# Performance work log

Hardware: AMD Instinct MI355X
Metric: run time of the kernel (lower is better)

The kernel has to match this reference:

```python
import jax, jax.numpy as jnp
import numpy as np

B, N, C = 16, 196608, 2

def setup_inputs() -> dict:
    key = jax.random.key(0)
    k1, k2, k3, k4, k5 = jax.random.split(key, 5)
    return {
        "r": jax.random.normal(k1, (B, N, C), dtype=jnp.float32),
        "w": jax.random.uniform(k2, (B, N, 2), dtype=jnp.float32),
        "J_p": jax.random.normal(k3, (B, N, C, 6), dtype=jnp.float32),
        "J_d": jax.random.uniform(k4, (B, N, C, 1), dtype=jnp.float32),
        "lmbda": jax.random.uniform(k5, (B, 1, 1), dtype=jnp.float32),
    }

def reference(r, w, J_p, J_d, lmbda):
    # r: (B,N,C)  w: (B,N,2)  J_p: (B,N,C,6)  J_d: (B,N,C,1)  lmbda: (B,1,1)
    conf = w[..., 0:1]                                  # (B,N,1)
    node_lambda = w[..., 1:2]                           # (B,N,1)
    conf4 = conf[..., None]                             # (B,N,1,1)
    Jd = J_d[..., 0]                                    # (B,N,C)

    # Gauss-Newton blocks (sum-over-N reductions of tiny outer products)
    H_pp = jnp.einsum('bnki,bnkj->bij', J_p, conf4 * J_p)        # (B,6,6)
    H_pd = jnp.einsum('bnki,bnkj->bnij', J_p, conf4 * J_d)       # (B,N,6,1)
    H_dd = jnp.einsum('bnk,bnk->bn', Jd, conf * Jd)[..., None]   # (B,N,1)
    wr = conf * r                                                # (B,N,C)
    g_p = jnp.einsum('bnki,bnk->bi', J_p, wr)[..., None]         # (B,6,1)
    g_d = jnp.einsum('bnk,bnk->bn', Jd, wr)[..., None]           # (B,N,1)

    eye6 = jnp.eye(6, dtype=H_pp.dtype)[None]                    # (1,6,6)
    H_pp = H_pp + lmbda * eye6                                   # LM damping on pose block

    # Depth block damping + safe inverse
    H_dd_safe = jnp.maximum(H_dd + lmbda + node_lambda, 1e-4)    # (B,N,1)
    inv_H_dd = 1.0 / H_dd_safe                                   # (B,N,1)

    # Schur complement: H_eff = H_pp - sum_n H_pd invHdd H_pd^T
    H_pd_invHdd = H_pd * inv_H_dd[..., None]                     # (B,N,6,1)
    term = jnp.einsum('bnik,bnjk->bij', H_pd_invHdd, H_pd)       # (B,6,6)
    H_eff = H_pp - term + (0.01 + 0.001) * eye6                  # eye*0.01 then ridge 0.001
    g_eff = g_p - jnp.sum(H_pd_invHdd * g_d[..., None], axis=1)  # (B,6,1)

    delta_pose = jnp.linalg.solve(H_eff, g_eff)                  # (B,6,1)
    dp = delta_pose[..., 0]                                      # (B,6)

    # Back-substitute depths
    v = jnp.einsum('bnij,bi->bnj', H_pd, dp)                     # (B,N,1)
    delta_depth = inv_H_dd * (g_d - v)                           # (B,N,1)

    delta_pose_out = jnp.clip(dp, -2.0, 2.0)                     # (B,6)
    return (delta_pose_out, delta_depth)
```

## Files before the change

### kernel.cpp

```cpp
#include <hip/hip_runtime.h>


constexpr int NACC = 27;

__device__ __forceinline__ void accum_point(
    float ja0, float ja1, float ja2, float ja3, float ja4, float ja5,
    float jb0, float jb1, float jb2, float jb3, float jb4, float jb5,
    float r0, float r1, float conf, float nlam, float jd0, float jd1,
    float lam, float* __restrict__ A, float* __restrict__ g)
{
    const float ja[6] = {ja0, ja1, ja2, ja3, ja4, ja5};
    const float jb[6] = {jb0, jb1, jb2, jb3, jb4, jb5};
    float h[6], gp[6];
#pragma unroll
    for (int i = 0; i < 6; ++i) {
        h[i]  = conf * (ja[i] * jd0 + jb[i] * jd1);
        gp[i] = conf * (ja[i] * r0 + jb[i] * r1);
    }
    const float hdd = conf * (jd0 * jd0 + jd1 * jd1);
    const float inv = 1.0f / fmaxf(hdd + lam + nlam, 1e-4f);
    const float gd  = conf * (jd0 * r0 + jd1 * r1);
    const float gdinv = gd * inv;
    int idx = 0;
#pragma unroll
    for (int i = 0; i < 6; ++i) {
        const float hii = h[i] * inv;
#pragma unroll
        for (int j = i; j < 6; ++j) {
            A[idx] += conf * (ja[i] * ja[j] + jb[i] * jb[j]) - hii * h[j];
            ++idx;
        }
        g[i] += gp[i] - h[i] * gdinv;
    }
}

__global__ __launch_bounds__(256) void dba_reduce(
    const float* __restrict__ r, const float* __restrict__ w,
    const float* __restrict__ J_p, const float* __restrict__ J_d,
    const float* __restrict__ lmbda, float* __restrict__ acc, int N)
{
    const int b = blockIdx.y;
    const float lam = lmbda[b];
    float A[21];
    float g[6];
#pragma unroll
    for (int i = 0; i < 21; ++i) A[i] = 0.f;
#pragma unroll
    for (int i = 0; i < 6; ++i) g[i] = 0.f;

    const size_t base = (size_t)b * (size_t)N;
    const int P = N >> 1;
    const int stride = gridDim.x * blockDim.x;
    for (int pr = blockIdx.x * blockDim.x + threadIdx.x; pr < P; pr += stride) {
        const size_t p = base + (size_t)(pr << 1);
        const float4 rv = *(const float4*)(r + p * 2);
        const float4 wv = *(const float4*)(w + p * 2);
        const float4 jd = *(const float4*)(J_d + p * 2);
        const float4* jp = (const float4*)(J_p + p * 12);
        const float4 q0 = jp[0];
        const float4 q1 = jp[1];
        const float4 q2 = jp[2];
        const float4 q3 = jp[3];
        const float4 q4 = jp[4];
        const float4 q5 = jp[5];

        accum_point(q0.x, q0.y, q0.z, q0.w, q1.x, q1.y,
                    q1.z, q1.w, q2.x, q2.y, q2.z, q2.w,
                    rv.x, rv.y, wv.x, wv.y, jd.x, jd.y, lam, A, g);
        accum_point(q3.x, q3.y, q3.z, q3.w, q4.x, q4.y,
                    q4.z, q4.w, q5.x, q5.y, q5.z, q5.w,
                    rv.z, rv.w, wv.z, wv.w, jd.z, jd.w, lam, A, g);
    }

    float v[NACC];
#pragma unroll
    for (int i = 0; i < 21; ++i) v[i] = A[i];
#pragma unroll
    for (int i = 0; i < 6; ++i) v[21 + i] = g[i];

#pragma unroll
    for (int off = 32; off > 0; off >>= 1) {
#pragma unroll
        for (int i = 0; i < NACC; ++i) v[i] += __shfl_down(v[i], off, 64);
    }

    __shared__ float sred[4][NACC];
    const int wave = threadIdx.x >> 6;
    const int lane = threadIdx.x & 63;
    if (lane == 0) {
#pragma unroll
        for (int i = 0; i < NACC; ++i) sred[wave][i] = v[i];
    }
    __syncthreads();
    if (threadIdx.x < NACC) {
        const float s = sred[0][threadIdx.x] + sred[1][threadIdx.x] +
                        sred[2][threadIdx.x] + sred[3][threadIdx.x];
        atomicAdd(&acc[b * 32 + threadIdx.x], s);
    }
}

__global__ void dba_solve(const float* __restrict__ acc,
                          const float* __restrict__ lmbda,
                          float* __restrict__ pose_out,
                          float* __restrict__ dp_ws, int B)
{
    const int b = blockIdx.x * blockDim.x + threadIdx.x;
    if (b >= B) return;
    float M[6][7];
    const float* a = acc + b * 32;
    int idx = 0;
#pragma unroll
    for (int i = 0; i < 6; ++i) {
#pragma unroll
        for (int j = i; j < 6; ++j) {
            const float t = a[idx++];
            M[i][j] = t;
            M[j][i] = t;
        }
    }
#pragma unroll
    for (int i = 0; i < 6; ++i) M[i][6] = a[21 + i];
    const float lam = lmbda[b];
#pragma unroll
    for (int i = 0; i < 6; ++i) M[i][i] += lam + 0.011f;

#pragma unroll
    for (int k = 0; k < 6; ++k) {
        const float piv = 1.0f / M[k][k];
#pragma unroll
        for (int j = 0; j < 7; ++j) M[k][j] *= piv;
#pragma unroll
        for (int i = 0; i < 6; ++i) {
            if (i == k) continue;
            const float f = M[i][k];
#pragma unroll
            for (int j = 0; j < 7; ++j) M[i][j] -= f * M[k][j];
        }
    }
#pragma unroll
    for (int i = 0; i < 6; ++i) {
        const float x = M[i][6];
        dp_ws[b * 6 + i] = x;
        pose_out[b * 6 + i] = fminf(fmaxf(x, -2.0f), 2.0f);
    }
}

__global__ __launch_bounds__(256) void dba_depth(
    const float* __restrict__ r, const float* __restrict__ w,
    const float* __restrict__ J_p, const float* __restrict__ J_d,
    const float* __restrict__ lmbda, const float* __restrict__ dp_ws,
    float* __restrict__ depth_out, int N)
{
    const int b = blockIdx.y;
    const float lam = lmbda[b];
    float dp[6];
#pragma unroll
    for (int i = 0; i < 6; ++i) dp[i] = dp_ws[b * 6 + i];

    const size_t base = (size_t)b * (size_t)N;
    const int P = N >> 1;
    const int stride = gridDim.x * blockDim.x;
    for (int pr = blockIdx.x * blockDim.x + threadIdx.x; pr < P; pr += stride) {
        const size_t p = base + (size_t)(pr << 1);
        const float4 rv = *(const float4*)(r + p * 2);
        const float4 wv = *(const float4*)(w + p * 2);
        const float4 jd = *(const float4*)(J_d + p * 2);
        const float4* jp = (const float4*)(J_p + p * 12);
        const float4 q0 = jp[0];
        const float4 q1 = jp[1];
        const float4 q2 = jp[2];
        const float4 q3 = jp[3];
        const float4 q4 = jp[4];
        const float4 q5 = jp[5];

        float2 outv;
        {
            const float ja[6] = {q0.x, q0.y, q0.z, q0.w, q1.x, q1.y};
            const float jb[6] = {q1.z, q1.w, q2.x, q2.y, q2.z, q2.w};
            float v = 0.f;
#pragma unroll
            for (int i = 0; i < 6; ++i)
                v += (ja[i] * jd.x + jb[i] * jd.y) * dp[i];
            v *= wv.x;
            const float hdd = wv.x * (jd.x * jd.x + jd.y * jd.y);
            const float inv = 1.0f / fmaxf(hdd + lam + wv.y, 1e-4f);
            const float gd  = wv.x * (jd.x * rv.x + jd.y * rv.y);
            outv.x = inv * (gd - v);
        }
        {
            const float ja[6] = {q3.x, q3.y, q3.z, q3.w, q4.x, q4.y};
            const float jb[6] = {q4.z, q4.w, q5.x, q5.y, q5.z, q5.w};
            float v = 0.f;
#pragma unroll
            for (int i = 0; i < 6; ++i)
                v += (ja[i] * jd.z + jb[i] * jd.w) * dp[i];
            v *= wv.z;
            const float hdd = wv.z * (jd.z * jd.z + jd.w * jd.w);
            const float inv = 1.0f / fmaxf(hdd + lam + wv.w, 1e-4f);
            const float gd  = wv.z * (jd.z * rv.z + jd.w * rv.w);
            outv.y = inv * (gd - v);
        }
        *(float2*)(depth_out + p) = outv;
    }
}

extern "C" void kernel_launch(void* const* d_in, const int* in_sizes, int n_in,
                              void* d_out, int out_size, void* d_ws, size_t ws_size,
                              hipStream_t stream)
{
    const float* r   = (const float*)d_in[0];
    const float* w   = (const float*)d_in[1];
    const float* J_p = (const float*)d_in[2];
    const float* J_d = (const float*)d_in[3];
    const float* lmb = (const float*)d_in[4];
    const int B = in_sizes[4];
    const int N = in_sizes[0] / (B * 2);

    float* acc   = (float*)d_ws;
    float* dp_ws = (float*)d_ws + B * 32;
    float* out   = (float*)d_out;

    hipMemsetAsync(acc, 0, B * 32 * sizeof(float), stream);

    dim3 grid(192, B);
    dba_reduce<<<grid, 256, 0, stream>>>(r, w, J_p, J_d, lmb, acc, N);
    dba_solve<<<1, 64, 0, stream>>>(acc, lmb, out, dp_ws, B);
    dba_depth<<<grid, 256, 0, stream>>>(r, w, J_p, J_d, lmb, dp_ws, out + B * 6, N);
}
```

Baseline: 307.0 us.

## Stage J_p through per-wave LDS transpose for coalesced loads in both passes

New measurement: 309.6 us. About the same (+0.8%).

```diff
diff --git a/kernel.cpp b/kernel.cpp
--- a/kernel.cpp
+++ b/kernel.cpp
@@ -4,13 +4,10 @@
 constexpr int NACC = 27;
 
 __device__ __forceinline__ void accum_point(
-    float ja0, float ja1, float ja2, float ja3, float ja4, float ja5,
-    float jb0, float jb1, float jb2, float jb3, float jb4, float jb5,
+    const float ja[6], const float jb[6],
     float r0, float r1, float conf, float nlam, float jd0, float jd1,
     float lam, float* __restrict__ A, float* __restrict__ g)
 {
-    const float ja[6] = {ja0, ja1, ja2, ja3, ja4, ja5};
-    const float jb[6] = {jb0, jb1, jb2, jb3, jb4, jb5};
     float h[6], gp[6];
 #pragma unroll
     for (int i = 0; i < 6; ++i) {
@@ -34,13 +31,27 @@
     }
 }
 
+constexpr int LDS_PITCH = 65;
+constexpr int LDS_WAVE  = 6 * LDS_PITCH;
+
+__device__ __forceinline__ void lds_fence()
+{
+    asm volatile("s_waitcnt lgkmcnt(0)" ::: "memory");
+    __builtin_amdgcn_sched_barrier(0);
+}
+
 __global__ __launch_bounds__(256) void dba_reduce(
     const float* __restrict__ r, const float* __restrict__ w,
     const float* __restrict__ J_p, const float* __restrict__ J_d,
     const float* __restrict__ lmbda, float* __restrict__ acc, int N)
 {
+    __shared__ float4 sJ[4][LDS_WAVE];
     const int b = blockIdx.y;
     const float lam = lmbda[b];
+    const int lane = threadIdx.x & 63;
+    const int wave = threadIdx.x >> 6;
+    float4* __restrict__ ldsW = sJ[wave];
+
     float A[21];
     float g[6];
 #pragma unroll
@@ -48,28 +59,71 @@
 #pragma unroll
     for (int i = 0; i < 6; ++i) g[i] = 0.f;
 
-    const size_t base = (size_t)b * (size_t)N;
-    const int P = N >> 1;
-    const int stride = gridDim.x * blockDim.x;
-    for (int pr = blockIdx.x * blockDim.x + threadIdx.x; pr < P; pr += stride) {
-        const size_t p = base + (size_t)(pr << 1);
-        const float4 rv = *(const float4*)(r + p * 2);
-        const float4 wv = *(const float4*)(w + p * 2);
-        const float4 jd = *(const float4*)(J_d + p * 2);
-        const float4* jp = (const float4*)(J_p + p * 12);
-        const float4 q0 = jp[0];
-        const float4 q1 = jp[1];
-        const float4 q2 = jp[2];
-        const float4 q3 = jp[3];
-        const float4 q4 = jp[4];
-        const float4 q5 = jp[5];
-
-        accum_point(q0.x, q0.y, q0.z, q0.w, q1.x, q1.y,
-                    q1.z, q1.w, q2.x, q2.y, q2.z, q2.w,
-                    rv.x, rv.y, wv.x, wv.y, jd.x, jd.y, lam, A, g);
-        accum_point(q3.x, q3.y, q3.z, q3.w, q4.x, q4.y,
-                    q4.z, q4.w, q5.x, q5.y, q5.z, q5.w,
-                    rv.z, rv.w, wv.z, wv.w, jd.z, jd.w, lam, A, g);
+    const size_t basePt = (size_t)b * (size_t)N;
+    const int P  = N >> 1;
+    const int PF = P & ~63;
+
+    const float4* __restrict__ r4  = (const float4*)r   + (basePt >> 1);
+    const float4* __restrict__ w4  = (const float4*)w   + (basePt >> 1);
+    const float4* __restrict__ jd4 = (const float4*)J_d + (basePt >> 1);
+    const float4* __restrict__ jp4 = (const float4*)J_p + basePt * 3;
+
+    const int gw = blockIdx.x * 4 + wave;
+    const int chunkStride = gridDim.x * 4;
+
+    for (int pr0 = gw << 6; pr0 < PF; pr0 += chunkStride << 6) {
+        const float4 rv = r4[pr0 + lane];
+        const float4 wv = w4[pr0 + lane];
+        const float4 jd = jd4[pr0 + lane];
+
+        const float4* __restrict__ jpseg = jp4 + (size_t)pr0 * 6;
+#pragma unroll
+        for (int k = 0; k < 6; ++k) {
+            const int gg = (k << 6) + lane;
+            const float4 q = jpseg[gg];
+            const int p = gg / 6;
+            const int s = gg - p * 6;
+            ldsW[s * LDS_PITCH + p] = q;
+        }
+        lds_fence();
+
+        {
+            const float4 J0 = ldsW[0 * LDS_PITCH + lane];
+            const float4 J1 = ldsW[1 * LDS_PITCH + lane];
+            const float4 J2 = ldsW[2 * LDS_PITCH + lane];
+            const float ja[6] = {J0.x, J0.y, J0.z, J0.w, J1.x, J1.y};
+            const float jb[6] = {J1.z, J1.w, J2.x, J2.y, J2.z, J2.w};
+            accum_point(ja, jb, rv.x, rv.y, wv.x, wv.y, jd.x, jd.y, lam, A, g);
+        }
+        {
+            const float4 J3 = ldsW[3 * LDS_PITCH + lane];
+            const float4 J4 = ldsW[4 * LDS_PITCH + lane];
+            const float4 J5 = ldsW[5 * LDS_PITCH + lane];
+            const float ja[6] = {J3.x, J3.y, J3.z, J3.w, J4.x, J4.y};
+            const float jb[6] = {J4.z, J4.w, J5.x, J5.y, J5.z, J5.w};
+            accum_point(ja, jb, rv.z, rv.w, wv.z, wv.w, jd.z, jd.w, lam, A, g);
+        }
+    }
+
+    for (int pr = PF + (int)(blockIdx.x * blockDim.x + threadIdx.x); pr < P;
+         pr += (int)(gridDim.x * blockDim.x)) {
+        const size_t pt = basePt + ((size_t)pr << 1);
+        const float4 rv = *(const float4*)(r + pt * 2);
+        const float4 wv = *(const float4*)(w + pt * 2);
+        const float4 jd = *(const float4*)(J_d + pt * 2);
+        const float4* jp = (const float4*)(J_p + pt * 12);
+        const float4 q0 = jp[0], q1 = jp[1], q2 = jp[2];
+        const float4 q3 = jp[3], q4 = jp[4], q5 = jp[5];
+        {
+            const float ja[6] = {q0.x, q0.y, q0.z, q0.w, q1.x, q1.y};
+            const float jb[6] = {q1.z, q1.w, q2.x, q2.y, q2.z, q2.w};
+            accum_point(ja, jb, rv.x, rv.y, wv.x, wv.y, jd.x, jd.y, lam, A, g);
+        }
+        {
+            const float ja[6] = {q3.x, q3.y, q3.z, q3.w, q4.x, q4.y};
+            const float jb[6] = {q4.z, q4.w, q5.x, q5.y, q5.z, q5.w};
+            accum_point(ja, jb, rv.z, rv.w, wv.z, wv.w, jd.z, jd.w, lam, A, g);
+        }
     }
 
     float v[NACC];
@@ -85,8 +139,6 @@
     }
 
     __shared__ float sred[4][NACC];
-    const int wave = threadIdx.x >> 6;
-    const int lane = threadIdx.x & 63;
     if (lane == 0) {
 #pragma unroll
         for (int i = 0; i < NACC; ++i) sred[wave][i] = v[i];
@@ -145,62 +197,108 @@
     }
 }
 
+__device__ __forceinline__ float depth_point(
+    const float ja[6], const float jb[6], const float* __restrict__ dp,
+    float r0, float r1, float conf, float nlam, float jd0, float jd1, float lam)
+{
+    float v = 0.f;
+#pragma unroll
+    for (int i = 0; i < 6; ++i)
+        v += (ja[i] * jd0 + jb[i] * jd1) * dp[i];
+    v *= conf;
+    const float hdd = conf * (jd0 * jd0 + jd1 * jd1);
+    const float inv = 1.0f / fmaxf(hdd + lam + nlam, 1e-4f);
+    const float gd  = conf * (jd0 * r0 + jd1 * r1);
+    return inv * (gd - v);
+}
+
 __global__ __launch_bounds__(256) void dba_depth(
     const float* __restrict__ r, const float* __restrict__ w,
     const float* __restrict__ J_p, const float* __restrict__ J_d,
     const float* __restrict__ lmbda, const float* __restrict__ dp_ws,
     float* __restrict__ depth_out, int N)
 {
+    __shared__ float4 sJ[4][LDS_WAVE];
     const int b = blockIdx.y;
     const float lam = lmbda[b];
+    const int lane = threadIdx.x & 63;
+    const int wave = threadIdx.x >> 6;
+    float4* __restrict__ ldsW = sJ[wave];
+
     float dp[6];
 #pragma unroll
     for (int i = 0; i < 6; ++i) dp[i] = dp_ws[b * 6 + i];
 
-    const size_t base = (size_t)b * (size_t)N;
-    const int P = N >> 1;
-    const int stride = gridDim.x * blockDim.x;
-    for (int pr = blockIdx.x * blockDim.x + threadIdx.x; pr < P; pr += stride) {
-        const size_t p = base + (size_t)(pr << 1);
-        const float4 rv = *(const float4*)(r + p * 2);
-        const float4 wv = *(const float4*)(w + p * 2);
-        const float4 jd = *(const float4*)(J_d + p * 2);
-        const float4* jp = (const float4*)(J_p + p * 12);
-        const float4 q0 = jp[0];
-        const float4 q1 = jp[1];
-        const float4 q2 = jp[2];
-        const float4 q3 = jp[3];
-        const float4 q4 = jp[4];
-        const float4 q5 = jp[5];
-
+    const size_t basePt = (size_t)b * (size_t)N;
+    const int P  = N >> 1;
+    const int PF = P & ~63;
+
+    const float4* __restrict__ r4  = (const float4*)r   + (basePt >> 1);
+    const float4* __restrict__ w4  = (const float4*)w   + (basePt >> 1);
+    const float4* __restrict__ jd4 = (const float4*)J_d + (basePt >> 1);
+    const float4* __restrict__ jp4 = (const float4*)J_p + basePt * 3;
+    float2* __restrict__ out2 = (float2*)depth_out + (basePt >> 1);
+
+    const int gw = blockIdx.x * 4 + wave;
+    const int chunkStride = gridDim.x * 4;
+
+    for (int pr0 = gw << 6; pr0 < PF; pr0 += chunkStride << 6) {
+        const float4 rv = r4[pr0 + lane];
+        const float4 wv = w4[pr0 + lane];
+        const float4 jd = jd4[pr0 + lane];
+
+        const float4* __restrict__ jpseg = jp4 + (size_t)pr0 * 6;
+#pragma unroll
+        for (int k = 0; k < 6; ++k) {
+            const int gg = (k << 6) + lane;
+            const float4 q = jpseg[gg];
+            const int p = gg / 6;
+            const int s = gg - p * 6;
+            ldsW[s * LDS_PITCH + p] = q;
+        }
+        lds_fence();
+
+        float2 outv;
+        {
+            const float4 J0 = ldsW[0 * LDS_PITCH + lane];
+            const float4 J1 = ldsW[1 * LDS_PITCH + lane];
+            const float4 J2 = ldsW[2 * LDS_PITCH + lane];
+            const float ja[6] = {J0.x, J0.y, J0.z, J0.w, J1.x, J1.y};
+            const float jb[6] = {J1.z, J1.w, J2.x, J2.y, J2.z, J2.w};
+            outv.x = depth_point(ja, jb, dp, rv.x, rv.y, wv.x, wv.y, jd.x, jd.y, lam);
+        }
+        {
+            const float4 J3 = ldsW[3 * LDS_PITCH + lane];
+            const float4 J4 = ldsW[4 * LDS_PITCH + lane];
+            const float4 J5 = ldsW[5 * LDS_PITCH + lane];
+            const float ja[6] = {J3.x, J3.y, J3.z, J3.w, J4.x, J4.y};
+            const float jb[6] = {J4.z, J4.w, J5.x, J5.y, J5.z, J5.w};
+            outv.y = depth_point(ja, jb, dp, rv.z, rv.w, wv.z, wv.w, jd.z, jd.w, lam);
+        }
+        out2[pr0 + lane] = outv;
+    }
+
+    for (int pr = PF + (int)(blockIdx.x * blockDim.x + threadIdx.x); pr < P;
+         pr += (int)(gridDim.x * blockDim.x)) {
+        const size_t pt = basePt + ((size_t)pr << 1);
+        const float4 rv = *(const float4*)(r + pt * 2);
+        const float4 wv = *(const float4*)(w + pt * 2);
+        const float4 jd = *(const float4*)(J_d + pt * 2);
+        const float4* jp = (const float4*)(J_p + pt * 12);
+        const float4 q0 = jp[0], q1 = jp[1], q2 = jp[2];
+        const float4 q3 = jp[3], q4 = jp[4], q5 = jp[5];
         float2 outv;
         {
             const float ja[6] = {q0.x, q0.y, q0.z, q0.w, q1.x, q1.y};
             const float jb[6] = {q1.z, q1.w, q2.x, q2.y, q2.z, q2.w};
-            float v = 0.f;
-#pragma unroll
-            for (int i = 0; i < 6; ++i)
-                v += (ja[i] * jd.x + jb[i] * jd.y) * dp[i];
-            v *= wv.x;
-            const float hdd = wv.x * (jd.x * jd.x + jd.y * jd.y);
-            const float inv = 1.0f / fmaxf(hdd + lam + wv.y, 1e-4f);
-            const float gd  = wv.x * (jd.x * rv.x + jd.y * rv.y);
-            outv.x = inv * (gd - v);
+            outv.x = depth_point(ja, jb, dp, rv.x, rv.y, wv.x, wv.y, jd.x, jd.y, lam);
         }
         {
             const float ja[6] = {q3.x, q3.y, q3.z, q3.w, q4.x, q4.y};
             const float jb[6] = {q4.z, q4.w, q5.x, q5.y, q5.z, q5.w};
-            float v = 0.f;
-#pragma unroll
-            for (int i = 0; i < 6; ++i)
-                v += (ja[i] * jd.z + jb[i] * jd.w) * dp[i];
-            v *= wv.z;
-            const float hdd = wv.z * (jd.z * jd.z + jd.w * jd.w);
-            const float inv = 1.0f / fmaxf(hdd + lam + wv.w, 1e-4f);
-            const float gd  = wv.z * (jd.z * rv.z + jd.w * rv.w);
-            outv.y = inv * (gd - v);
-        }
-        *(float2*)(depth_out + p) = outv;
+            outv.y = depth_point(ja, jb, dp, rv.z, rv.w, wv.z, wv.w, jd.z, jd.w, lam);
+        }
+        *(float2*)(depth_out + pt) = outv;
     }
 }
 
@@ -222,7 +320,7 @@
 
     hipMemsetAsync(acc, 0, B * 32 * sizeof(float), stream);
 
-    dim3 grid(192, B);
+    dim3 grid(96, B);
     dba_reduce<<<grid, 256, 0, stream>>>(r, w, J_p, J_d, lmb, acc, N);
     dba_solve<<<1, 64, 0, stream>>>(acc, lmb, out, dp_ws, B);
     dba_depth<<<grid, 256, 0, stream>>>(r, w, J_p, J_d, lmb, dp_ws, out + B * 6, N);
```

## Fuse reduce, solve and depth back-substitution into one cooperative kernel with register caching

Applied to the files above, without the earlier changes.

Measured after the change: 618.3 us. +101.4%, slower.

```diff
diff --git a/kernel.cpp b/kernel.cpp
--- a/kernel.cpp
+++ b/kernel.cpp
@@ -1,16 +1,21 @@
 #include <hip/hip_runtime.h>
-
+#include <hip/hip_cooperative_groups.h>
+
+namespace cg = cooperative_groups;
+
+
+using f4 = __attribute__((ext_vector_type(4))) float;
+using f2 = __attribute__((ext_vector_type(2))) float;
 
 constexpr int NACC = 27;
+constexpr int CHUNKS = 12;
 
 __device__ __forceinline__ void accum_point(
-    float ja0, float ja1, float ja2, float ja3, float ja4, float ja5,
-    float jb0, float jb1, float jb2, float jb3, float jb4, float jb5,
+    const float ja[6], const float jb[6],
     float r0, float r1, float conf, float nlam, float jd0, float jd1,
-    float lam, float* __restrict__ A, float* __restrict__ g)
-{
-    const float ja[6] = {ja0, ja1, ja2, ja3, ja4, ja5};
-    const float jb[6] = {jb0, jb1, jb2, jb3, jb4, jb5};
+    float lam, float* __restrict__ A, float* __restrict__ g,
+    float* __restrict__ c7)
+{
     float h[6], gp[6];
 #pragma unroll
     for (int i = 0; i < 6; ++i) {
@@ -21,10 +26,12 @@
     const float inv = 1.0f / fmaxf(hdd + lam + nlam, 1e-4f);
     const float gd  = conf * (jd0 * r0 + jd1 * r1);
     const float gdinv = gd * inv;
+    c7[6] = gdinv;
     int idx = 0;
 #pragma unroll
     for (int i = 0; i < 6; ++i) {
         const float hii = h[i] * inv;
+        c7[i] = hii;
 #pragma unroll
         for (int j = i; j < 6; ++j) {
             A[idx] += conf * (ja[i] * ja[j] + jb[i] * jb[j]) - hii * h[j];
@@ -34,7 +41,158 @@
     }
 }
 
-__global__ __launch_bounds__(256) void dba_reduce(
+__device__ __forceinline__ void solve6(const float* __restrict__ a, float lam,
+                                       float* __restrict__ pose,
+                                       float* __restrict__ dp)
+{
+    float M[6][7];
+    int idx = 0;
+#pragma unroll
+    for (int i = 0; i < 6; ++i) {
+#pragma unroll
+        for (int j = i; j < 6; ++j) {
+            const float t = a[idx++];
+            M[i][j] = t;
+            M[j][i] = t;
+        }
+    }
+#pragma unroll
+    for (int i = 0; i < 6; ++i) M[i][6] = a[21 + i];
+#pragma unroll
+    for (int i = 0; i < 6; ++i) M[i][i] += lam + 0.011f;
+
+#pragma unroll
+    for (int k = 0; k < 6; ++k) {
+        const float piv = 1.0f / M[k][k];
+#pragma unroll
+        for (int j = 0; j < 7; ++j) M[k][j] *= piv;
+#pragma unroll
+        for (int i = 0; i < 6; ++i) {
+            if (i == k) continue;
+            const float f = M[i][k];
+#pragma unroll
+            for (int j = 0; j < 7; ++j) M[i][j] -= f * M[k][j];
+        }
+    }
+#pragma unroll
+    for (int i = 0; i < 6; ++i) {
+        const float x = M[i][6];
+        dp[i] = x;
+        pose[i] = fminf(fmaxf(x, -2.0f), 2.0f);
+    }
+}
+
+__global__ __launch_bounds__(256, 2) void dba_fused(
+    const float* __restrict__ r, const float* __restrict__ w,
+    const float* __restrict__ J_p, const float* __restrict__ J_d,
+    const float* __restrict__ lmbda, float* __restrict__ acc,
+    float* __restrict__ dp_ws, float* __restrict__ pose_out,
+    float* __restrict__ depth_out, int N)
+{
+    const int b  = blockIdx.x >> 5;
+    const int bb = blockIdx.x & 31;
+    const int tid_b = (bb << 8) + threadIdx.x;
+    const float lam = lmbda[b];
+
+    const size_t basePt = (size_t)b * (size_t)N;
+    const f4* __restrict__ r4  = (const f4*)r   + (basePt >> 1);
+    const f4* __restrict__ w4  = (const f4*)w   + (basePt >> 1);
+    const f4* __restrict__ jd4 = (const f4*)J_d + (basePt >> 1);
+    const f4* __restrict__ jp4 = (const f4*)J_p + basePt * 3;
+    f2* __restrict__ out2 = (f2*)depth_out + (basePt >> 1);
+
+    float A[21];
+    float g[6];
+#pragma unroll
+    for (int i = 0; i < 21; ++i) A[i] = 0.f;
+#pragma unroll
+    for (int i = 0; i < 6; ++i) g[i] = 0.f;
+
+    float ca[CHUNKS][7];
+    float cb[CHUNKS][7];
+
+#pragma unroll
+    for (int it = 0; it < CHUNKS; ++it) {
+        const int pr = tid_b + it * 8192;
+        const f4 rv = r4[pr];
+        const f4 wv = w4[pr];
+        const f4 jd = jd4[pr];
+        const f4* jp = jp4 + (size_t)pr * 6;
+        const f4 q0 = jp[0];
+        const f4 q1 = jp[1];
+        const f4 q2 = jp[2];
+        const f4 q3 = jp[3];
+        const f4 q4 = jp[4];
+        const f4 q5 = jp[5];
+        {
+            const float ja[6] = {q0[0], q0[1], q0[2], q0[3], q1[0], q1[1]};
+            const float jb[6] = {q1[2], q1[3], q2[0], q2[1], q2[2], q2[3]};
+            accum_point(ja, jb, rv[0], rv[1], wv[0], wv[1], jd[0], jd[1],
+                        lam, A, g, ca[it]);
+        }
+        {
+            const float ja[6] = {q3[0], q3[1], q3[2], q3[3], q4[0], q4[1]};
+            const float jb[6] = {q4[2], q4[3], q5[0], q5[1], q5[2], q5[3]};
+            accum_point(ja, jb, rv[2], rv[3], wv[2], wv[3], jd[2], jd[3],
+                        lam, A, g, cb[it]);
+        }
+    }
+
+    {
+        float v[NACC];
+#pragma unroll
+        for (int i = 0; i < 21; ++i) v[i] = A[i];
+#pragma unroll
+        for (int i = 0; i < 6; ++i) v[21 + i] = g[i];
+#pragma unroll
+        for (int off = 32; off > 0; off >>= 1) {
+#pragma unroll
+            for (int i = 0; i < NACC; ++i) v[i] += __shfl_down(v[i], off, 64);
+        }
+        __shared__ float sred[4][NACC];
+        const int wave = threadIdx.x >> 6;
+        const int lane = threadIdx.x & 63;
+        if (lane == 0) {
+#pragma unroll
+            for (int i = 0; i < NACC; ++i) sred[wave][i] = v[i];
+        }
+        __syncthreads();
+        if (threadIdx.x < NACC) {
+            const float s = sred[0][threadIdx.x] + sred[1][threadIdx.x] +
+                            sred[2][threadIdx.x] + sred[3][threadIdx.x];
+            atomicAdd(&acc[b * 32 + threadIdx.x], s);
+        }
+    }
+
+    __threadfence();
+    cg::this_grid().sync();
+
+    if (blockIdx.x < 16 && threadIdx.x == 0) {
+        const int sb = blockIdx.x;
+        solve6(acc + sb * 32, lmbda[sb], pose_out + sb * 6, dp_ws + sb * 6);
+    }
+    __threadfence();
+    cg::this_grid().sync();
+
+    float dp[6];
+#pragma unroll
+    for (int i = 0; i < 6; ++i) dp[i] = dp_ws[b * 6 + i];
+
+#pragma unroll
+    for (int it = 0; it < CHUNKS; ++it) {
+        const int pr = tid_b + it * 8192;
+        f2 o;
+        o[0] = ca[it][6] - (ca[it][0] * dp[0] + ca[it][1] * dp[1] +
+                            ca[it][2] * dp[2] + ca[it][3] * dp[3] +
+                            ca[it][4] * dp[4] + ca[it][5] * dp[5]);
+        o[1] = cb[it][6] - (cb[it][0] * dp[0] + cb[it][1] * dp[1] +
+                            cb[it][2] * dp[2] + cb[it][3] * dp[3] +
+                            cb[it][4] * dp[4] + cb[it][5] * dp[5]);
+        out2[pr] = o;
+    }
+}
+
+__global__ __launch_bounds__(256) void dba_reduce_fb(
     const float* __restrict__ r, const float* __restrict__ w,
     const float* __restrict__ J_p, const float* __restrict__ J_d,
     const float* __restrict__ lmbda, float* __restrict__ acc, int N)
@@ -48,28 +206,34 @@
 #pragma unroll
     for (int i = 0; i < 6; ++i) g[i] = 0.f;
 
-    const size_t base = (size_t)b * (size_t)N;
+    const size_t basePt = (size_t)b * (size_t)N;
     const int P = N >> 1;
-    const int stride = gridDim.x * blockDim.x;
-    for (int pr = blockIdx.x * blockDim.x + threadIdx.x; pr < P; pr += stride) {
-        const size_t p = base + (size_t)(pr << 1);
-        const float4 rv = *(const float4*)(r + p * 2);
-        const float4 wv = *(const float4*)(w + p * 2);
-        const float4 jd = *(const float4*)(J_d + p * 2);
-        const float4* jp = (const float4*)(J_p + p * 12);
-        const float4 q0 = jp[0];
-        const float4 q1 = jp[1];
-        const float4 q2 = jp[2];
-        const float4 q3 = jp[3];
-        const float4 q4 = jp[4];
-        const float4 q5 = jp[5];
-
-        accum_point(q0.x, q0.y, q0.z, q0.w, q1.x, q1.y,
-                    q1.z, q1.w, q2.x, q2.y, q2.z, q2.w,
-                    rv.x, rv.y, wv.x, wv.y, jd.x, jd.y, lam, A, g);
-        accum_point(q3.x, q3.y, q3.z, q3.w, q4.x, q4.y,
-                    q4.z, q4.w, q5.x, q5.y, q5.z, q5.w,
-                    rv.z, rv.w, wv.z, wv.w, jd.z, jd.w, lam, A, g);
+    const f4* __restrict__ r4  = (const f4*)r   + (basePt >> 1);
+    const f4* __restrict__ w4  = (const f4*)w   + (basePt >> 1);
+    const f4* __restrict__ jd4 = (const f4*)J_d + (basePt >> 1);
+    const f4* __restrict__ jp4 = (const f4*)J_p + basePt * 3;
+
+    float c7a[7], c7b[7];
+    for (int pr = blockIdx.x * blockDim.x + threadIdx.x; pr < P;
+         pr += gridDim.x * blockDim.x) {
+        const f4 rv = r4[pr];
+        const f4 wv = w4[pr];
+        const f4 jd = jd4[pr];
+        const f4* jp = jp4 + (size_t)pr * 6;
+        const f4 q0 = jp[0], q1 = jp[1], q2 = jp[2];
+        const f4 q3 = jp[3], q4 = jp[4], q5 = jp[5];
+        {
+            const float ja[6] = {q0[0], q0[1], q0[2], q0[3], q1[0], q1[1]};
+            const float jb[6] = {q1[2], q1[3], q2[0], q2[1], q2[2], q2[3]};
+            accum_point(ja, jb, rv[0], rv[1], wv[0], wv[1], jd[0], jd[1],
+                        lam, A, g, c7a);
+        }
+        {
+            const float ja[6] = {q3[0], q3[1], q3[2], q3[3], q4[0], q4[1]};
+            const float jb[6] = {q4[2], q4[3], q5[0], q5[1], q5[2], q5[3]};
+            accum_point(ja, jb, rv[2], rv[3], wv[2], wv[3], jd[2], jd[3],
+                        lam, A, g, c7b);
+        }
     }
 
     float v[NACC];
@@ -77,13 +241,11 @@
     for (int i = 0; i < 21; ++i) v[i] = A[i];
 #pragma unroll
     for (int i = 0; i < 6; ++i) v[21 + i] = g[i];
-
 #pragma unroll
     for (int off = 32; off > 0; off >>= 1) {
 #pragma unroll
         for (int i = 0; i < NACC; ++i) v[i] += __shfl_down(v[i], off, 64);
     }
-
     __shared__ float sred[4][NACC];
     const int wave = threadIdx.x >> 6;
     const int lane = threadIdx.x & 63;
@@ -99,53 +261,17 @@
     }
 }
 
-__global__ void dba_solve(const float* __restrict__ acc,
-                          const float* __restrict__ lmbda,
-                          float* __restrict__ pose_out,
-                          float* __restrict__ dp_ws, int B)
+__global__ void dba_solve_fb(const float* __restrict__ acc,
+                             const float* __restrict__ lmbda,
+                             float* __restrict__ pose_out,
+                             float* __restrict__ dp_ws, int B)
 {
     const int b = blockIdx.x * blockDim.x + threadIdx.x;
     if (b >= B) return;
-    float M[6][7];
-    const float* a = acc + b * 32;
-    int idx = 0;
-#pragma unroll
-    for (int i = 0; i < 6; ++i) {
-#pragma unroll
-        for (int j = i; j < 6; ++j) {
-            const float t = a[idx++];
-            M[i][j] = t;
-            M[j][i] = t;
-        }
-    }
-#pragma unroll
-    for (int i = 0; i < 6; ++i) M[i][6] = a[21 + i];
-    const float lam = lmbda[b];
-#pragma unroll
-    for (int i = 0; i < 6; ++i) M[i][i] += lam + 0.011f;
-
-#pragma unroll
-    for (int k = 0; k < 6; ++k) {
-        const float piv = 1.0f / M[k][k];
-#pragma unroll
-        for (int j = 0; j < 7; ++j) M[k][j] *= piv;
-#pragma unroll
-        for (int i = 0; i < 6; ++i) {
-            if (i == k) continue;
-            const float f = M[i][k];
-#pragma unroll
-            for (int j = 0; j < 7; ++j) M[i][j] -= f * M[k][j];
-        }
-    }
-#pragma unroll
-    for (int i = 0; i < 6; ++i) {
-        const float x = M[i][6];
-        dp_ws[b * 6 + i] = x;
-        pose_out[b * 6 + i] = fminf(fmaxf(x, -2.0f), 2.0f);
-    }
-}
-
-__global__ __launch_bounds__(256) void dba_depth(
+    solve6(acc + b * 32, lmbda[b], pose_out + b * 6, dp_ws + b * 6);
+}
+
+__global__ __launch_bounds__(256) void dba_depth_fb(
     const float* __restrict__ r, const float* __restrict__ w,
     const float* __restrict__ J_p, const float* __restrict__ J_d,
     const float* __restrict__ lmbda, const float* __restrict__ dp_ws,
@@ -157,50 +283,50 @@
 #pragma unroll
     for (int i = 0; i < 6; ++i) dp[i] = dp_ws[b * 6 + i];
 
-    const size_t base = (size_t)b * (size_t)N;
+    const size_t basePt = (size_t)b * (size_t)N;
     const int P = N >> 1;
-    const int stride = gridDim.x * blockDim.x;
-    for (int pr = blockIdx.x * blockDim.x + threadIdx.x; pr < P; pr += stride) {
-        const size_t p = base + (size_t)(pr << 1);
-        const float4 rv = *(const float4*)(r + p * 2);
-        const float4 wv = *(const float4*)(w + p * 2);
-        const float4 jd = *(const float4*)(J_d + p * 2);
-        const float4* jp = (const float4*)(J_p + p * 12);
-        const float4 q0 = jp[0];
-        const float4 q1 = jp[1];
-        const float4 q2 = jp[2];
-        const float4 q3 = jp[3];
-        const float4 q4 = jp[4];
-        const float4 q5 = jp[5];
-
-        float2 outv;
-        {
-            const float ja[6] = {q0.x, q0.y, q0.z, q0.w, q1.x, q1.y};
-            const float jb[6] = {q1.z, q1.w, q2.x, q2.y, q2.z, q2.w};
+    const f4* __restrict__ r4  = (const f4*)r   + (basePt >> 1);
+    const f4* __restrict__ w4  = (const f4*)w   + (basePt >> 1);
+    const f4* __restrict__ jd4 = (const f4*)J_d + (basePt >> 1);
+    const f4* __restrict__ jp4 = (const f4*)J_p + basePt * 3;
+    f2* __restrict__ out2 = (f2*)depth_out + (basePt >> 1);
+
+    for (int pr = blockIdx.x * blockDim.x + threadIdx.x; pr < P;
+         pr += gridDim.x * blockDim.x) {
+        const f4 rv = r4[pr];
+        const f4 wv = w4[pr];
+        const f4 jd = jd4[pr];
+        const f4* jp = jp4 + (size_t)pr * 6;
+        const f4 q0 = jp[0], q1 = jp[1], q2 = jp[2];
+        const f4 q3 = jp[3], q4 = jp[4], q5 = jp[5];
+        f2 o;
+        {
+            const float ja[6] = {q0[0], q0[1], q0[2], q0[3], q1[0], q1[1]};
+            const float jb[6] = {q1[2], q1[3], q2[0], q2[1], q2[2], q2[3]};
             float v = 0.f;
 #pragma unroll
             for (int i = 0; i < 6; ++i)
-                v += (ja[i] * jd.x + jb[i] * jd.y) * dp[i];
-            v *= wv.x;
-            const float hdd = wv.x * (jd.x * jd.x + jd.y * jd.y);
-            const float inv = 1.0f / fmaxf(hdd + lam + wv.y, 1e-4f);
-            const float gd  = wv.x * (jd.x * rv.x + jd.y * rv.y);
-            outv.x = inv * (gd - v);
-        }
-        {
-            const float ja[6] = {q3.x, q3.y, q3.z, q3.w, q4.x, q4.y};
-            const float jb[6] = {q4.z, q4.w, q5.x, q5.y, q5.z, q5.w};
+                v += (ja[i] * jd[0] + jb[i] * jd[1]) * dp[i];
+            v *= wv[0];
+            const float hdd = wv[0] * (jd[0] * jd[0] + jd[1] * jd[1]);
+            const float inv = 1.0f / fmaxf(hdd + lam + wv[1], 1e-4f);
+            const float gd  = wv[0] * (jd[0] * rv[0] + jd[1] * rv[1]);
+            o[0] = inv * (gd - v);
+        }
+        {
+            const float ja[6] = {q3[0], q3[1], q3[2], q3[3], q4[0], q4[1]};
+            const float jb[6] = {q4[2], q4[3], q5[0], q5[1], q5[2], q5[3]};
             float v = 0.f;
 #pragma unroll
             for (int i = 0; i < 6; ++i)
-                v += (ja[i] * jd.z + jb[i] * jd.w) * dp[i];
-            v *= wv.z;
-            const float hdd = wv.z * (jd.z * jd.z + jd.w * jd.w);
-            const float inv = 1.0f / fmaxf(hdd + lam + wv.w, 1e-4f);
-            const float gd  = wv.z * (jd.z * rv.z + jd.w * rv.w);
-            outv.y = inv * (gd - v);
-        }
-        *(float2*)(depth_out + p) = outv;
+                v += (ja[i] * jd[2] + jb[i] * jd[3]) * dp[i];
+            v *= wv[2];
+            const float hdd = wv[2] * (jd[2] * jd[2] + jd[3] * jd[3]);
+            const float inv = 1.0f / fmaxf(hdd + lam + wv[3], 1e-4f);
+            const float gd  = wv[2] * (jd[2] * rv[2] + jd[3] * rv[3]);
+            o[1] = inv * (gd - v);
+        }
+        out2[pr] = o;
     }
 }
 
@@ -217,13 +343,35 @@
     const int N = in_sizes[0] / (B * 2);
 
     float* acc   = (float*)d_ws;
-    float* dp_ws = (float*)d_ws + B * 32;
+    float* dp_ws = (float*)d_ws + 512;
     float* out   = (float*)d_out;
+    float* pose  = out;
+    float* depth = out + B * 6;
 
     hipMemsetAsync(acc, 0, B * 32 * sizeof(float), stream);
 
+    static int coop = -1;
+    if (coop < 0) {
+        int dev = 0, v = 0;
+        hipGetDevice(&dev);
+        hipDeviceGetAttribute(&v, hipDeviceAttributeCooperativeLaunch, dev);
+        coop = v;
+    }
+
+    if (coop && B == 16 && N == 196608) {
+        int n = N;
+        void* args[] = {(void*)&r,   (void*)&w,     (void*)&J_p,
+                        (void*)&J_d, (void*)&lmb,   (void*)&acc,
+                        (void*)&dp_ws, (void*)&pose, (void*)&depth,
+                        (void*)&n};
+        hipError_t e = hipLaunchCooperativeKernel(
+            (const void*)dba_fused, dim3(512), dim3(256), args, 0, stream);
+        if (e == hipSuccess) return;
+    }
+
     dim3 grid(192, B);
-    dba_reduce<<<grid, 256, 0, stream>>>(r, w, J_p, J_d, lmb, acc, N);
-    dba_solve<<<1, 64, 0, stream>>>(acc, lmb, out, dp_ws, B);
-    dba_depth<<<grid, 256, 0, stream>>>(r, w, J_p, J_d, lmb, dp_ws, out + B * 6, N);
-}
+    dba_reduce_fb<<<grid, 256, 0, stream>>>(r, w, J_p, J_d, lmb, acc, N);
+    dba_solve_fb<<<1, 64, 0, stream>>>(acc, lmb, pose, dp_ws, B);
+    dba_depth_fb<<<grid, 256, 0, stream>>>(r, w, J_p, J_d, lmb, dp_ws,
+                                           depth, N);
+}
```
